# Kernel tuning notes

Measured on AMD Instinct MI355X. Metric: run time of the kernel, lower is better.

## Reference

```python
import jax, jax.numpy as jnp
import numpy as np

N = 50000       # number of nodes
E = 800000      # number of edges (avg degree 16)
F_IN = 128      # in_features
F_OUT = 128     # out_features
EPS = 1e-5      # BatchNorm1d default eps


def setup_inputs() -> dict:
    key = jax.random.key(0)
    k = jax.random.split(key, 4)
    x = jax.random.normal(k[0], (N, F_IN), dtype=jnp.float32)
    src = jax.random.randint(k[1], (E,), 0, N, dtype=jnp.int32)
    dst = jax.random.randint(k[2], (E,), 0, N, dtype=jnp.int32)
    # row-normalized adjacency weights (mean aggregation): 1 / in-degree(dst)
    deg = jax.ops.segment_sum(jnp.ones((E,), jnp.float32), dst, num_segments=N)
    w_edge = (1.0 / jnp.maximum(deg, 1.0))[dst]
    # Linear(2*F_IN -> F_OUT, bias=False) weight, torch layout [out, in]
    W = jax.random.normal(k[3], (F_OUT, 2 * F_IN), dtype=jnp.float32) * 0.05
    gamma = jnp.ones((F_OUT,), jnp.float32)
    beta = jnp.zeros((F_OUT,), jnp.float32)
    return {"x": x, "src": src, "dst": dst, "w_edge": w_edge,
            "W": W, "gamma": gamma, "beta": beta}


def reference(x, src, dst, w_edge, W, gamma, beta):
    # spmm(adj, x): gather source features, scale by edge weight, scatter-add to dst
    msgs = w_edge[:, None] * x[src]                       # [E, F_IN]
    agg = jax.ops.segment_sum(msgs, dst, num_segments=N)  # [N, F_IN]
    h = jnp.concatenate([x, agg], axis=1)                 # [N, 2*F_IN]
    y = h @ W.T                                           # [N, F_OUT]
    # BatchNorm1d in training mode: batch stats over node dim, biased variance
    mean = jnp.mean(y, axis=0)
    var = jnp.mean((y - mean) ** 2, axis=0)
    out = (y - mean) * jax.lax.rsqrt(var + EPS) * gamma + beta
    return out
```

## Files before the change

kernel.cpp:

```cpp
#include <hip/hip_runtime.h>

#define F 128
#define EPSV 1e-5f
#define NPB 256
#define CAP 5120

typedef _Float16 f16x8 __attribute__((ext_vector_type(8)));
typedef _Float16 f16x4 __attribute__((ext_vector_type(4)));
typedef _Float16 f16x2 __attribute__((ext_vector_type(2)));
typedef float    f32x4 __attribute__((ext_vector_type(4)));

#define SRCMASK 0x1FFFFFF

__global__ __launch_bounds__(256) void k_phase0(
        const float* __restrict__ x, _Float16* __restrict__ xh, int n4x,
        const float* __restrict__ W, _Float16* __restrict__ wh, int n4w,
        const int* __restrict__ dst, int* __restrict__ histA,
        int E, int Epb, int NF, int nbx) {
    int t = threadIdx.x, b = blockIdx.x;
    if (b < NPB) {
        __shared__ int h[512];
        h[t] = 0; h[t + 256] = 0;
        __syncthreads();
        int beg = b * Epb;
        int end = min(beg + Epb, E);
        for (int i = beg + t; i < end; i += 256)
            atomicAdd(&h[dst[i] >> 7], 1);
        __syncthreads();
        for (int f = t; f < NF; f += 256)
            histA[f * NPB + b] = h[f];
    } else if (b < NPB + nbx) {
        int i = (b - NPB) * 256 + t;
        if (i >= n4x) return;
        float4 v = *reinterpret_cast<const float4*>(x + (size_t)i * 4);
        f16x4 o = { (_Float16)v.x, (_Float16)v.y, (_Float16)v.z, (_Float16)v.w };
        *reinterpret_cast<f16x4*>(xh + (size_t)i * 4) = o;
    } else {
        int i = (b - NPB - nbx) * 256 + t;
        if (i >= n4w) return;
        float4 v = *reinterpret_cast<const float4*>(W + (size_t)i * 4);
        f16x4 o = { (_Float16)v.x, (_Float16)v.y, (_Float16)v.z, (_Float16)v.w };
        *reinterpret_cast<f16x4*>(wh + (size_t)i * 4) = o;
    }
}

__global__ __launch_bounds__(256) void k_pa2a(
        const int* __restrict__ histA, int* __restrict__ cursorRel,
        int* __restrict__ tot) {
    __shared__ int wsum[4];
    int f = blockIdx.x, t = threadIdx.x;
    int lane = t & 63, wv = t >> 6;
    int v = histA[f * NPB + t];
    int sc = v;
    #pragma unroll
    for (int off = 1; off < 64; off <<= 1) {
        int o = __shfl_up(sc, off);
        if (lane >= off) sc += o;
    }
    if (lane == 63) wsum[wv] = sc;
    __syncthreads();
    int woff = 0;
    for (int i = 0; i < wv; ++i) woff += wsum[i];
    cursorRel[f * NPB + t] = woff + sc - v;
    if (t == 255) tot[f] = woff + sc;
}

__global__ __launch_bounds__(256) void k_pa2b(
        const int* __restrict__ tot, int* __restrict__ bktptr,
        float* __restrict__ stats, int NF) {
    int t = threadIdx.x;
    stats[t] = 0.f;
    if (t < 64) {
        int carry = 0;
        for (int base = 0; base < NF; base += 64) {
            int i = base + t;
            int v = (i < NF) ? tot[i] : 0;
            int sc = v;
            #pragma unroll
            for (int off = 1; off < 64; off <<= 1) {
                int o = __shfl_up(sc, off);
                if (t >= off) sc += o;
            }
            if (i < NF) bktptr[i] = carry + sc - v;
            carry += __shfl(sc, 63);
        }
        if (t == 0) bktptr[NF] = carry;
    }
}

__global__ __launch_bounds__(256) void k_pa3(
        const int* __restrict__ dst, const int* __restrict__ src,
        const float* __restrict__ we, const int* __restrict__ cursorRel,
        const int* __restrict__ bktptr,
        int2* __restrict__ payload, int E, int Epb, int NF) {
    __shared__ int cur[512];
    int t = threadIdx.x, b = blockIdx.x;
    for (int f = t; f < NF; f += 256)
        cur[f] = bktptr[f] + cursorRel[f * NPB + b];
    __syncthreads();
    int beg = b * Epb;
    int end = min(beg + Epb, E);
    for (int i0 = beg + t * 4; i0 < end; i0 += 1024) {
        int d[4], s[4]; float w[4];
        if (i0 + 3 < end) {
            int4   d4 = *reinterpret_cast<const int4*>(dst + i0);
            int4   s4 = *reinterpret_cast<const int4*>(src + i0);
            float4 w4 = *reinterpret_cast<const float4*>(we + i0);
            d[0] = d4.x; d[1] = d4.y; d[2] = d4.z; d[3] = d4.w;
            s[0] = s4.x; s[1] = s4.y; s[2] = s4.z; s[3] = s4.w;
            w[0] = w4.x; w[1] = w4.y; w[2] = w4.z; w[3] = w4.w;
        } else {
            #pragma unroll
            for (int u = 0; u < 4; ++u) {
                int i = min(i0 + u, E - 1);
                d[u] = dst[i]; s[u] = src[i]; w[u] = we[i];
            }
        }
        int slot[4];
        #pragma unroll
        for (int u = 0; u < 4; ++u)
            if (i0 + u < end) slot[u] = atomicAdd(&cur[d[u] >> 7], 1);
        #pragma unroll
        for (int u = 0; u < 4; ++u)
            if (i0 + u < end)
                payload[slot[u]] = make_int2(s[u] | ((d[u] & 127) << 25),
                                             __float_as_int(w[u]));
    }
}

__global__ __launch_bounds__(512) void k_sortagg(
        const _Float16* __restrict__ xh, const int* __restrict__ bktptr,
        const int2* __restrict__ payload, _Float16* __restrict__ aggh, int N) {
    __shared__ int2 pl[CAP];
    __shared__ int h[128], hs[129], cur[128];
    int t = threadIdx.x, f = blockIdx.x;
    int beg = bktptr[f], end = bktptr[f + 1];
    int cnt = min(end - beg, CAP);
    if (t < 128) h[t] = 0;
    __syncthreads();
    for (int i = t; i < cnt; i += 512)
        atomicAdd(&h[(payload[beg + i].x >> 25) & 127], 1);
    __syncthreads();
    if (t < 64) {
        int v0 = h[t], s0 = v0;
        #pragma unroll
        for (int off = 1; off < 64; off <<= 1) {
            int o = __shfl_up(s0, off);
            if (t >= off) s0 += o;
        }
        int tot0 = __shfl(s0, 63);
        hs[t] = s0 - v0;
        int v1 = h[64 + t], s1 = v1;
        #pragma unroll
        for (int off = 1; off < 64; off <<= 1) {
            int o = __shfl_up(s1, off);
            if (t >= off) s1 += o;
        }
        hs[64 + t] = tot0 + s1 - v1;
    }
    __syncthreads();
    if (t < 128) cur[t] = hs[t];
    if (t == 128) hs[128] = cnt;
    __syncthreads();
    for (int i = t; i < cnt; i += 512) {
        int2 p = payload[beg + i];
        int r = (p.x >> 25) & 127;
        int pos = atomicAdd(&cur[r], 1);
        pl[pos] = p;
    }
    __syncthreads();

    int wv = t >> 6, lane = t & 63;
    int row0 = f << 7;
    #pragma unroll 1
    for (int k = 0; k < 16; ++k) {
        int r = wv * 16 + k;
        int n = row0 + r;
        if (n >= N) break;
        int b0 = hs[r], b1 = hs[r + 1];
        float ax = 0.f, ay = 0.f;
        for (int i = b0; i < b1; i += 8) {
            int2 p[8];
            #pragma unroll
            for (int u = 0; u < 8; ++u)
                p[u] = pl[min(i + u, b1 - 1)];
            f16x2 v[8];
            #pragma unroll
            for (int u = 0; u < 8; ++u)
                v[u] = *reinterpret_cast<const f16x2*>(
                    xh + (size_t)(p[u].x & SRCMASK) * F + lane * 2);
            #pragma unroll
            for (int u = 0; u < 8; ++u) {
                float wu = (i + u < b1) ? __int_as_float(p[u].y) : 0.f;
                ax += wu * (float)v[u][0];
                ay += wu * (float)v[u][1];
            }
        }
        f16x2 o = { (_Float16)ax, (_Float16)ay };
        *reinterpret_cast<f16x2*>(aggh + (size_t)n * F + lane * 2) = o;
    }
}

__global__ __launch_bounds__(512) void k_gemm_mfma(
        const _Float16* __restrict__ xh, const _Float16* __restrict__ aggh,
        const _Float16* __restrict__ wh, _Float16* __restrict__ yh,
        float* __restrict__ colsum, float* __restrict__ colsumsq, int N) {
    __shared__ _Float16 lds_w[32768];
    __shared__ float lds_s[8][128], lds_q[8][128];
    int t = threadIdx.x, w = t >> 6, l = t & 63;
    int lo16 = l & 15, hi4 = l >> 4;

    #pragma unroll
    for (int i = 0; i < 8; ++i) {
        int c = i * 512 + t;
        int o = c >> 5, kc = c & 31;
        f16x8 v = *reinterpret_cast<const f16x8*>(wh + (size_t)c * 8);
        int byte = (o * 512 + kc * 16) ^ ((o & 7) << 4);
        *reinterpret_cast<f16x8*>((char*)lds_w + byte) = v;
    }
    __syncthreads();

    int rows0 = blockIdx.x * 128 + w * 16;
    int ra0 = rows0 + lo16;
    if (ra0 >= N) ra0 = N - 1;

    f32x4 acc0[8] = {};
    #pragma unroll
    for (int kb = 0; kb < 8; ++kb) {
        const _Float16* base = (kb < 4) ? xh : aggh;
        int koff = (kb & 3) * 32 + hi4 * 8;
        f16x8 a0 = *reinterpret_cast<const f16x8*>(base + (size_t)ra0 * F + koff);
        #pragma unroll
        for (int ct = 0; ct < 8; ++ct) {
            int o = ct * 16 + lo16;
            int byte = (o * 512 + kb * 64 + hi4 * 16) ^ ((o & 7) << 4);
            f16x8 b = *reinterpret_cast<const f16x8*>((char*)lds_w + byte);
            acc0[ct] = __builtin_amdgcn_mfma_f32_16x16x32_f16(a0, b, acc0[ct], 0, 0, 0);
        }
    }

    #pragma unroll
    for (int ct = 0; ct < 8; ++ct) {
        float sv = 0.f, qv = 0.f;
        int col = ct * 16 + lo16;
        #pragma unroll
        for (int r = 0; r < 4; ++r) {
            int row0 = rows0 + hi4 * 4 + r;
            float v0 = acc0[ct][r];
            if (row0 < N) {
                yh[(size_t)row0 * F + col] = (_Float16)v0;
                sv += v0; qv += v0 * v0;
            }
        }
        sv += __shfl_xor(sv, 16); sv += __shfl_xor(sv, 32);
        qv += __shfl_xor(qv, 16); qv += __shfl_xor(qv, 32);
        if (l < 16) {
            lds_s[w][col] = sv;
            lds_q[w][col] = qv;
        }
    }
    __syncthreads();
    if (t < 128) {
        float S = 0.f, Q = 0.f;
        #pragma unroll
        for (int wv = 0; wv < 8; ++wv) {
            S += lds_s[wv][t];
            Q += lds_q[wv][t];
        }
        atomicAdd(&colsum[t], S);
        atomicAdd(&colsumsq[t], Q);
    }
}

__global__ __launch_bounds__(256) void k_norm(
        const _Float16* __restrict__ yh, float* __restrict__ out,
        const float* __restrict__ colsum, const float* __restrict__ colsumsq,
        const float* __restrict__ gamma, const float* __restrict__ beta,
        float ninv, int total8) {
    __shared__ float sc_sh[F], sh_sh[F];
    int t = threadIdx.x;
    if (t < F) {
        float mean = colsum[t] * ninv;
        float var = colsumsq[t] * ninv - mean * mean;
        float rstd = rsqrtf(var + EPSV);
        float sc = gamma[t] * rstd;
        sc_sh[t] = sc;
        sh_sh[t] = beta[t] - mean * sc;
    }
    __syncthreads();
    int idx = blockIdx.x * 256 + t;
    if (idx >= total8) return;
    int col8 = (idx & 15) * 8;
    f16x8 v = *reinterpret_cast<const f16x8*>(yh + (size_t)idx * 8);
    float4 o0, o1;
    o0.x = (float)v[0] * sc_sh[col8 + 0] + sh_sh[col8 + 0];
    o0.y = (float)v[1] * sc_sh[col8 + 1] + sh_sh[col8 + 1];
    o0.z = (float)v[2] * sc_sh[col8 + 2] + sh_sh[col8 + 2];
    o0.w = (float)v[3] * sc_sh[col8 + 3] + sh_sh[col8 + 3];
    o1.x = (float)v[4] * sc_sh[col8 + 4] + sh_sh[col8 + 4];
    o1.y = (float)v[5] * sc_sh[col8 + 5] + sh_sh[col8 + 5];
    o1.z = (float)v[6] * sc_sh[col8 + 6] + sh_sh[col8 + 6];
    o1.w = (float)v[7] * sc_sh[col8 + 7] + sh_sh[col8 + 7];
    *reinterpret_cast<float4*>(out + (size_t)idx * 8)     = o0;
    *reinterpret_cast<float4*>(out + (size_t)idx * 8 + 4) = o1;
}

extern "C" void kernel_launch(void* const* d_in, const int* in_sizes, int n_in,
                              void* d_out, int out_size, void* d_ws, size_t ws_size,
                              hipStream_t stream) {
    (void)n_in; (void)out_size; (void)ws_size;
    const float* x     = (const float*)d_in[0];
    const int*   src   = (const int*)d_in[1];
    const int*   dst   = (const int*)d_in[2];
    const float* we    = (const float*)d_in[3];
    const float* W     = (const float*)d_in[4];
    const float* gamma = (const float*)d_in[5];
    const float* beta  = (const float*)d_in[6];
    int N = in_sizes[0] / F;
    int E = in_sizes[1];

    int NF  = (N + 127) / 128;
    int Epb = (((E + NPB - 1) / NPB) + 3) & ~3;

    char* ws = (char*)d_ws;
    size_t off = 0;
    auto alloc = [&](size_t bytes) {
        void* p = ws + off;
        off += (bytes + 255) & ~(size_t)255;
        return p;
    };
    _Float16* xh     = (_Float16*)alloc((size_t)N * F * sizeof(_Float16));
    _Float16* aggh   = (_Float16*)alloc((size_t)N * F * sizeof(_Float16));
    _Float16* yh     = (_Float16*)alloc((size_t)N * F * sizeof(_Float16));
    _Float16* wh     = (_Float16*)alloc((size_t)F * 2 * F * sizeof(_Float16));
    float* stats     = (float*)alloc(2 * F * sizeof(float));
    int*   histA     = (int*)alloc((size_t)512 * NPB * sizeof(int));
    int*   cursorRel = (int*)alloc((size_t)512 * NPB * sizeof(int));
    int*   tot       = (int*)alloc((size_t)512 * sizeof(int));
    int*   bktptr    = (int*)alloc((size_t)(512 + 1) * sizeof(int));
    int2*  payload   = (int2*)alloc((size_t)E * sizeof(int2));
    float* colsum    = stats;
    float* colsumsq  = stats + F;

    float* y = (float*)d_out;

    int n4x = N * F / 4, n4w = 2 * F * F / 4;
    int nbx = (n4x + 255) / 256, nbw = (n4w + 255) / 256;
    hipLaunchKernelGGL(k_phase0, dim3(NPB + nbx + nbw), dim3(256), 0, stream,
                       x, xh, n4x, W, wh, n4w, dst, histA, E, Epb, NF, nbx);

    hipLaunchKernelGGL(k_pa2a, dim3(NF), dim3(256), 0, stream,
                       histA, cursorRel, tot);
    hipLaunchKernelGGL(k_pa2b, dim3(1), dim3(256), 0, stream,
                       tot, bktptr, stats, NF);
    hipLaunchKernelGGL(k_pa3, dim3(NPB), dim3(256), 0, stream,
                       dst, src, we, cursorRel, bktptr, payload, E, Epb, NF);

    hipLaunchKernelGGL(k_sortagg, dim3(NF), dim3(512), 0, stream,
                       xh, bktptr, payload, aggh, N);

    hipLaunchKernelGGL(k_gemm_mfma, dim3((N + 127) / 128), dim3(512), 0, stream,
                       xh, aggh, wh, yh, colsum, colsumsq, N);

    hipLaunchKernelGGL(k_norm, dim3((N * F / 8 + 255) / 256), dim3(256), 0, stream,
                       yh, y, colsum, colsumsq, gamma, beta, 1.0f / (float)N, N * F / 8);
}
```

Baseline: 92.00 us.

## Fuse sorted aggregation with MFMA GEMM, keeping aggregated tile in LDS

Merges the per-bucket aggregation kernel and the MFMA GEMM kernel into one kernel. Each block aggregates its 128 destination nodes into a swizzled LDS tile and feeds that tile straight into the GEMM, along with the LDS-resident weights. This removes the global write and re-read of the fp16 aggregate buffer and one kernel launch. In exchange LDS use per block rises sharply (weights, aggregate tile and payload together), which may lower occupancy during the gather-heavy aggregation phase.

```diff
diff --git a/kernel.cpp b/kernel.cpp
--- a/kernel.cpp
+++ b/kernel.cpp
@@ -128,12 +128,27 @@
     }
 }
 
-__global__ __launch_bounds__(512) void k_sortagg(
+__global__ __launch_bounds__(512) void k_fuse(
         const _Float16* __restrict__ xh, const int* __restrict__ bktptr,
-        const int2* __restrict__ payload, _Float16* __restrict__ aggh, int N) {
+        const int2* __restrict__ payload, const _Float16* __restrict__ wh,
+        _Float16* __restrict__ yh, float* __restrict__ colsum,
+        float* __restrict__ colsumsq, int N) {
+    __shared__ _Float16 lds_w[32768];
+    __shared__ _Float16 agg_lds[16384];
     __shared__ int2 pl[CAP];
     __shared__ int h[128], hs[129], cur[128];
+    __shared__ float lds_s[8][128], lds_q[8][128];
     int t = threadIdx.x, f = blockIdx.x;
+
+    #pragma unroll
+    for (int i = 0; i < 8; ++i) {
+        int c = i * 512 + t;
+        int o = c >> 5, kc = c & 31;
+        f16x8 v = *reinterpret_cast<const f16x8*>(wh + (size_t)c * 8);
+        int byte = (o * 512 + kc * 16) ^ ((o & 7) << 4);
+        *reinterpret_cast<f16x8*>((char*)lds_w + byte) = v;
+    }
+
     int beg = bktptr[f], end = bktptr[f + 1];
     int cnt = min(end - beg, CAP);
     if (t < 128) h[t] = 0;
@@ -196,40 +211,30 @@
                 ay += wu * (float)v[u][1];
             }
         }
-        f16x2 o = { (_Float16)ax, (_Float16)ay };
-        *reinterpret_cast<f16x2*>(aggh + (size_t)n * F + lane * 2) = o;
-    }
-}
-
-__global__ __launch_bounds__(512) void k_gemm_mfma(
-        const _Float16* __restrict__ xh, const _Float16* __restrict__ aggh,
-        const _Float16* __restrict__ wh, _Float16* __restrict__ yh,
-        float* __restrict__ colsum, float* __restrict__ colsumsq, int N) {
-    __shared__ _Float16 lds_w[32768];
-    __shared__ float lds_s[8][128], lds_q[8][128];
-    int t = threadIdx.x, w = t >> 6, l = t & 63;
+        f16x2 o2 = { (_Float16)ax, (_Float16)ay };
+        int byte = (r * 256 + lane * 4) ^ ((r & 7) << 4);
+        *reinterpret_cast<f16x2*>((char*)agg_lds + byte) = o2;
+    }
+    __syncthreads();
+
+    int l = lane;
     int lo16 = l & 15, hi4 = l >> 4;
-
-    #pragma unroll
-    for (int i = 0; i < 8; ++i) {
-        int c = i * 512 + t;
-        int o = c >> 5, kc = c & 31;
-        f16x8 v = *reinterpret_cast<const f16x8*>(wh + (size_t)c * 8);
-        int byte = (o * 512 + kc * 16) ^ ((o & 7) << 4);
-        *reinterpret_cast<f16x8*>((char*)lds_w + byte) = v;
-    }
-    __syncthreads();
-
-    int rows0 = blockIdx.x * 128 + w * 16;
+    int rows0 = row0 + wv * 16;
+    int rloc = wv * 16 + lo16;
     int ra0 = rows0 + lo16;
     if (ra0 >= N) ra0 = N - 1;
 
     f32x4 acc0[8] = {};
     #pragma unroll
     for (int kb = 0; kb < 8; ++kb) {
-        const _Float16* base = (kb < 4) ? xh : aggh;
-        int koff = (kb & 3) * 32 + hi4 * 8;
-        f16x8 a0 = *reinterpret_cast<const f16x8*>(base + (size_t)ra0 * F + koff);
+        f16x8 a0;
+        if (kb < 4) {
+            a0 = *reinterpret_cast<const f16x8*>(
+                xh + (size_t)ra0 * F + kb * 32 + hi4 * 8);
+        } else {
+            int byte = (rloc * 256 + (kb & 3) * 64 + hi4 * 16) ^ ((rloc & 7) << 4);
+            a0 = *reinterpret_cast<const f16x8*>((char*)agg_lds + byte);
+        }
         #pragma unroll
         for (int ct = 0; ct < 8; ++ct) {
             int o = ct * 16 + lo16;
@@ -245,27 +250,27 @@
         int col = ct * 16 + lo16;
         #pragma unroll
         for (int r = 0; r < 4; ++r) {
-            int row0 = rows0 + hi4 * 4 + r;
+            int row = rows0 + hi4 * 4 + r;
             float v0 = acc0[ct][r];
-            if (row0 < N) {
-                yh[(size_t)row0 * F + col] = (_Float16)v0;
+            if (row < N) {
+                yh[(size_t)row * F + col] = (_Float16)v0;
                 sv += v0; qv += v0 * v0;
             }
         }
         sv += __shfl_xor(sv, 16); sv += __shfl_xor(sv, 32);
         qv += __shfl_xor(qv, 16); qv += __shfl_xor(qv, 32);
         if (l < 16) {
-            lds_s[w][col] = sv;
-            lds_q[w][col] = qv;
+            lds_s[wv][col] = sv;
+            lds_q[wv][col] = qv;
         }
     }
     __syncthreads();
     if (t < 128) {
         float S = 0.f, Q = 0.f;
         #pragma unroll
-        for (int wv = 0; wv < 8; ++wv) {
-            S += lds_s[wv][t];
-            Q += lds_q[wv][t];
+        for (int w8 = 0; w8 < 8; ++w8) {
+            S += lds_s[w8][t];
+            Q += lds_q[w8][t];
         }
         atomicAdd(&colsum[t], S);
         atomicAdd(&colsumsq[t], Q);
@@ -330,7 +335,6 @@
         return p;
     };
     _Float16* xh     = (_Float16*)alloc((size_t)N * F * sizeof(_Float16));
-    _Float16* aggh   = (_Float16*)alloc((size_t)N * F * sizeof(_Float16));
     _Float16* yh     = (_Float16*)alloc((size_t)N * F * sizeof(_Float16));
     _Float16* wh     = (_Float16*)alloc((size_t)F * 2 * F * sizeof(_Float16));
     float* stats     = (float*)alloc(2 * F * sizeof(float));
@@ -356,11 +360,8 @@
     hipLaunchKernelGGL(k_pa3, dim3(NPB), dim3(256), 0, stream,
                        dst, src, we, cursorRel, bktptr, payload, E, Epb, NF);
 
-    hipLaunchKernelGGL(k_sortagg, dim3(NF), dim3(512), 0, stream,
-                       xh, bktptr, payload, aggh, N);
-
-    hipLaunchKernelGGL(k_gemm_mfma, dim3((N + 127) / 128), dim3(512), 0, stream,
-                       xh, aggh, wh, yh, colsum, colsumsq, N);
+    hipLaunchKernelGGL(k_fuse, dim3(NF), dim3(512), 0, stream,
+                       xh, bktptr, payload, wh, yh, colsum, colsumsq, N);
 
     hipLaunchKernelGGL(k_norm, dim3((N * F / 8 + 255) / 256), dim3(256), 0, stream,
                        yh, y, colsum, colsumsq, gamma, beta, 1.0f / (float)N, N * F / 8);
```

Result: slower. 105.4 us (+14.6%).
